# Performance work log

Measured on AMD Instinct MI355X. Metric: run time of the kernel, lower is better.

## Reference

```python
import jax, jax.numpy as jnp
import numpy as np

S, B, E, H, NQ, V, T = 128, 128, 64, 8, 8, 30000, 12
N_RAND_OPS = 30


def _build_random_layer(n_wires, n_ops=N_RAND_OPS, seed=1234):
    # Deterministic stand-in for tq.RandomLayer(n_ops=30): random fixed-angle
    # rotations and CNOTs over the wires.
    rng = np.random.RandomState(seed)
    ops = []
    for _ in range(n_ops):
        kind = rng.randint(4)
        if kind == 3 and n_wires >= 2:
            c = int(rng.randint(n_wires))
            t = int(rng.randint(n_wires - 1))
            if t >= c:
                t += 1
            ops.append(('cnot', c, t, 0.0))
        else:
            g = ('rx', 'ry', 'rz')[kind % 3]
            ops.append((g, int(rng.randint(n_wires)), -1, float(rng.uniform(0.0, 2 * np.pi))))
    return ops

_RAND_OPS = _build_random_layer(H)


def _apply_rot(state, kind, theta, w):
    # state: (N, 2, 2, ..., 2); wire w lives on axis w+1. theta: scalar or (N,).
    th = jnp.asarray(theta, jnp.float32)
    if th.ndim == 1:
        th = th.reshape((-1,) + (1,) * (state.ndim - 2))
    th = th / 2
    a0 = jnp.take(state, 0, axis=w + 1)
    a1 = jnp.take(state, 1, axis=w + 1)
    c, s = jnp.cos(th), jnp.sin(th)
    if kind == 'rx':
        n0, n1 = c * a0 - 1j * s * a1, -1j * s * a0 + c * a1
    elif kind == 'ry':
        n0, n1 = c * a0 - s * a1, s * a0 + c * a1
    else:  # rz
        p = jnp.exp(-1j * th)
        n0, n1 = p * a0, jnp.conj(p) * a1
    return jnp.stack([n0, n1], axis=w + 1)


def _apply_cnot(state, c, t):
    s0 = jnp.take(state, 0, axis=c + 1)
    s1 = jnp.take(state, 1, axis=c + 1)
    t_ax = t + 1 if t < c else t  # target axis after removing control axis
    s1 = jnp.flip(s1, axis=t_ax)
    return jnp.stack([s0, s1], axis=c + 1)


def _measure_z(state):
    probs = jnp.real(state * jnp.conj(state))
    n = state.ndim - 1
    zs = []
    for w in range(n):
        d = jnp.take(probs, 0, axis=w + 1) - jnp.take(probs, 1, axis=w + 1)
        zs.append(d.sum(axis=tuple(range(1, d.ndim))))
    return jnp.stack(zs, axis=1)  # (N, n_wires)


def setup_inputs() -> dict:
    key = jax.random.key(0)
    ks = jax.random.split(key, 10)
    fan_lin = E + H
    return {
        'emb': jax.random.normal(ks[0], (V, E), jnp.float32),
        'Win': jax.random.normal(ks[1], (4, NQ, fan_lin), jnp.float32) / np.sqrt(fan_lin),
        'b_in': jax.random.normal(ks[2], (4, NQ), jnp.float32) * 0.1,
        'phi': jax.random.uniform(ks[3], (4, NQ), jnp.float32, 0.0, 2 * np.pi),
        'Wout': jax.random.normal(ks[4], (4, H, NQ), jnp.float32) / np.sqrt(NQ),
        'b_out': jax.random.normal(ks[5], (4, H), jnp.float32) * 0.1,
        'phiq': jax.random.uniform(ks[6], (H,), jnp.float32, 0.0, 2 * np.pi),
        'Whead': jax.random.normal(ks[7], (T, H), jnp.float32) / np.sqrt(H),
        'b_head': jax.random.normal(ks[8], (T,), jnp.float32) * 0.1,
        'sentence': jax.random.randint(ks[9], (S, B), 0, V, jnp.int64),
    }


def reference(emb, Win, b_in, phi, Wout, b_out, phiq, Whead, b_head, sentence):
    embeds = emb[sentence]  # (S, B, E)
    bsz = sentence.shape[1]
    h0 = jnp.zeros((bsz, H), emb.dtype)
    c0 = jnp.zeros_like(h0)

    def step(carry, x):
        hx, cx = carry
        comb = jnp.concatenate([x, hx], axis=1)  # (B, E+H)
        # QGate closed form: RX(z_i) encode + trainable RX(phi_i) + CNOT chain
        # gives <Z_k> = prod_{j<=k} cos(z_j + phi_j).
        z = jnp.einsum('bf,gqf->bgq', comb, Win) + b_in + phi  # (B,4,NQ)
        q = jnp.cumprod(jnp.cos(z), axis=-1)
        pre = jnp.einsum('bgq,ghq->bgh', q, Wout) + b_out      # (B,4,H)
        f = jax.nn.sigmoid(pre[:, 0])
        i = jax.nn.sigmoid(pre[:, 1])
        g = jnp.tanh(pre[:, 2])
        o = jax.nn.sigmoid(pre[:, 3])
        cx = f * cx + i * g
        hx = o * jnp.tanh(cx)
        return (hx, cx), hx

    _, outs = jax.lax.scan(step, (h0, c0), embeds)  # (S, B, H)
    flat = outs.transpose(1, 0, 2).reshape(-1, H)   # (B*S, H) batch-major (as in source)

    # QFC head: statevector simulation over H wires
    n = H
    N = flat.shape[0]
    state = jnp.zeros((N, 2 ** n), jnp.complex64).at[:, 0].set(1.0)
    state = state.reshape((N,) + (2,) * n)
    for w in range(n):
        state = _apply_rot(state, 'ry', flat[:, w], w)
    for name, a, b, ang in _RAND_OPS:
        if name == 'cnot':
            state = _apply_cnot(state, a, b)
        else:
            state = _apply_rot(state, name, ang, a)
    for w in range(n):
        state = _apply_rot(state, 'rx', phiq[w], w)
    zexp = _measure_z(state)                        # (B*S, H)
    logits = zexp @ Whead.T + b_head
    # faithful to source: view batch-major flat tensor as (seq, batch, T)
    logits = logits.reshape(S, B, T)
    return jax.nn.log_softmax(logits, axis=2)
```

## Files before the change

kernel.cpp:

```cpp
#include <hip/hip_runtime.h>
#include <math.h>
#include <stdint.h>

#define S_    128
#define B_    128
#define E_    64
#define H_    8
#define T_    12
#define FAN_  72
#define NOPS_ 30
#define MAXG_ 30

constexpr double CT_PI = 3.14159265358979323846;

constexpr double ct_cos(double x) {
    double t = 1.0, s = 1.0, x2 = x * x;
    for (int k = 1; k <= 20; k++) { t *= -x2 / ((2.0*k - 1.0) * (2.0*k)); s += t; }
    return s;
}
constexpr double ct_sin(double x) {
    double t = x, s = x, x2 = x * x;
    for (int k = 1; k <= 20; k++) { t *= -x2 / ((2.0*k) * (2.0*k + 1.0)); s += t; }
    return s;
}

constexpr void ct_mmul(const double* A, const double* B, double* C) {
    for (int i = 0; i < 2; i++)
        for (int j = 0; j < 2; j++) {
            double rr = 0.0, ii = 0.0;
            for (int k = 0; k < 2; k++) {
                double ar = A[(i*2+k)*2], ai = A[(i*2+k)*2+1];
                double br = B[(k*2+j)*2], bi = B[(k*2+j)*2+1];
                rr += ar*br - ai*bi;
                ii += ar*bi + ai*br;
            }
            C[(i*2+j)*2] = rr; C[(i*2+j)*2+1] = ii;
        }
}

struct CTC {
    int n;
    int type[MAXG_];
    int w1[MAXG_];
    int w2[MAXG_];
    double U[MAXG_][8];
    double initM[8][8];
    double endM[8][8];
};

constexpr CTC build_ct() {
    uint32_t mt[624] = {};
    int idx = 624;
    {
        uint32_t s = 1234u;
        for (int i = 0; i < 624; i++) {
            mt[i] = s;
            s = 1812433253u * (s ^ (s >> 30)) + (uint32_t)i + 1u;
        }
    }
    auto nextf = [&]() -> uint32_t {
        if (idx >= 624) {
            for (int i = 0; i < 624; i++) {
                uint32_t y = (mt[i] & 0x80000000u) | (mt[(i+1)%624] & 0x7fffffffu);
                uint32_t v = mt[(i+397)%624] ^ (y >> 1);
                mt[i] = (y & 1u) ? (v ^ 0x9908b0dfu) : v;
            }
            idx = 0;
        }
        uint32_t y = mt[idx++];
        y ^= y >> 11;
        y ^= (y << 7)  & 0x9d2c5680u;
        y ^= (y << 15) & 0xefc60000u;
        y ^= y >> 18;
        return y;
    };
    auto randint = [&](uint32_t n) -> uint32_t {
        uint32_t rng = n - 1u, mask = rng;
        mask |= mask >> 1; mask |= mask >> 2; mask |= mask >> 4;
        mask |= mask >> 8; mask |= mask >> 16;
        uint32_t v = 0;
        do { v = nextf() & mask; } while (v > rng);
        return v;
    };
    auto uniform2pi = [&]() -> double {
        uint32_t a = nextf() >> 5;
        uint32_t b = nextf() >> 6;
        double d = ((double)a * 67108864.0 + (double)b) / 9007199254740992.0;
        return 2.0 * CT_PI * d;
    };

    int kindA[NOPS_] = {}, aA[NOPS_] = {}, bA[NOPS_] = {};
    double UA[NOPS_][8] = {};
    for (int i = 0; i < NOPS_; i++) {
        uint32_t kind = randint(4);
        if (kind == 3u) {
            int c = (int)randint(8);
            int t = (int)randint(7);
            if (t >= c) t += 1;
            kindA[i] = 1; aA[i] = c; bA[i] = t;
            UA[i][0] = 1.0; UA[i][6] = 1.0;
        } else {
            int g = (int)(kind % 3u);
            int w = (int)randint(8);
            double th = uniform2pi();
            double c = ct_cos(0.5 * th), s = ct_sin(0.5 * th);
            kindA[i] = 0; aA[i] = w; bA[i] = -1;
            if (g == 0)      { UA[i][0]=c;  UA[i][3]=-s; UA[i][5]=-s; UA[i][6]=c; }
            else if (g == 1) { UA[i][0]=c;  UA[i][2]=-s; UA[i][4]= s; UA[i][6]=c; }
            else             { UA[i][0]=c;  UA[i][1]=-s; UA[i][6]= c; UA[i][7]=s; }
        }
    }

    int ikind[MAXG_] = {}, ia[MAXG_] = {}, ib[MAXG_] = {};
    double iU[MAXG_][8] = {};
    int cnt = 0;
    double initM[8][8] = {}, endM[8][8] = {};
    for (int w = 0; w < 8; w++) { initM[w][0] = 1.0; initM[w][6] = 1.0;
                                  endM[w][0]  = 1.0; endM[w][6]  = 1.0; }

    for (int oi = 0; oi < NOPS_; oi++) {
        if (kindA[oi] == 0) {
            int w = aA[oi], k = cnt - 1;
            bool merged = false;
            while (k >= 0) {
                if (ikind[k] == 0) {
                    if (ia[k] == w) {
                        double tmp[8] = {};
                        ct_mmul(UA[oi], iU[k], tmp);
                        for (int j = 0; j < 8; j++) iU[k][j] = tmp[j];
                        merged = true; break;
                    }
                    k--;
                } else {
                    if (w == ia[k] || w == ib[k]) break;
                    k--;
                }
            }
            if (merged) continue;
            if (k < 0) {
                double tmp[8] = {};
                ct_mmul(UA[oi], initM[w], tmp);
                for (int j = 0; j < 8; j++) initM[w][j] = tmp[j];
                continue;
            }
            ikind[cnt] = 0; ia[cnt] = w; ib[cnt] = -1;
            for (int j = 0; j < 8; j++) iU[cnt][j] = UA[oi][j];
            cnt++;
        } else {
            int c = aA[oi], t2 = bA[oi], k = cnt - 1;
            bool cancelled = false;
            while (k >= 0) {
                if (ikind[k] == 0) {
                    int w = ia[k];
                    if (w == c || w == t2) break;
                    k--;
                } else {
                    int c2 = ia[k], tt = ib[k];
                    if (c2 == c && tt == t2) {
                        for (int m = k; m < cnt - 1; m++) {
                            ikind[m] = ikind[m+1]; ia[m] = ia[m+1]; ib[m] = ib[m+1];
                            for (int j = 0; j < 8; j++) iU[m][j] = iU[m+1][j];
                        }
                        cnt--; cancelled = true; break;
                    }
                    if (c2 != t2 && tt != c) k--;
                    else break;
                }
            }
            if (!cancelled) {
                ikind[cnt] = 1; ia[cnt] = c; ib[cnt] = t2;
                for (int j = 0; j < 8; j++) iU[cnt][j] = 0.0;
                iU[cnt][0] = 1.0; iU[cnt][6] = 1.0;
                cnt++;
            }
        }
    }
    bool blocked[8] = {};
    for (int k = cnt - 1; k >= 0; k--) {
        if (ikind[k] == 0) {
            int w = ia[k];
            if (!blocked[w]) {
                double tmp[8] = {};
                ct_mmul(endM[w], iU[k], tmp);
                for (int j = 0; j < 8; j++) endM[w][j] = tmp[j];
                for (int m = k; m < cnt - 1; m++) {
                    ikind[m] = ikind[m+1]; ia[m] = ia[m+1]; ib[m] = ib[m+1];
                    for (int j = 0; j < 8; j++) iU[m][j] = iU[m+1][j];
                }
                cnt--;
            }
        } else {
            blocked[ia[k]] = true; blocked[ib[k]] = true;
        }
    }

    CTC q = {};
    q.n = cnt;
    for (int i = 0; i < cnt; i++) {
        q.type[i] = ikind[i]; q.w1[i] = ia[i]; q.w2[i] = ib[i];
        for (int j = 0; j < 8; j++) q.U[i][j] = iU[i][j];
    }
    for (int w = 0; w < 8; w++)
        for (int j = 0; j < 8; j++) { q.initM[w][j] = initM[w][j]; q.endM[w][j] = endM[w][j]; }
    return q;
}

constexpr CTC CIRC = build_ct();

__device__ __forceinline__ float sigmoid_f(float x) { return 1.f / (1.f + __expf(-x)); }
__device__ __forceinline__ float tanh_f(float x) {
    float e = __expf(2.f * x);
    return 1.f - 2.f / (e + 1.f);
}

template<int CTRL>
__device__ __forceinline__ float dppf(float x) {
    union { float f; int i; } u, r;
    u.f = x;
    r.i = __builtin_amdgcn_update_dpp(0, u.i, CTRL, 0xF, 0xF, true);
    return r.f;
}

template<int M>
__device__ __forceinline__ float lane_xor(float x, int lane) {
    if constexpr (M == 1)  return dppf<0xB1>(x);
    else if constexpr (M == 2) return dppf<0x4E>(x);
    else if constexpr (M == 4) {
        float a = dppf<0x104>(x);
        float b = dppf<0x114>(x);
        return (lane & 4) ? b : a;
    }
    else if constexpr (M == 8) return dppf<0x128>(x);
    else return __shfl_xor(x, M, 64);
}

template<int W>
__device__ __forceinline__ float exch(float x, int lane) {
    if constexpr (W == 0) return __shfl_xor(x, 32, 64);
    else if constexpr (W == 1) return __shfl_xor(x, 16, 64);
    else if constexpr (W == 2) return lane_xor<8>(x, lane);
    else if constexpr (W == 3) return lane_xor<4>(x, lane);
    else if constexpr (W == 4) return lane_xor<2>(x, lane);
    else return lane_xor<1>(x, lane);
}

template<int W>
__device__ __forceinline__ int qbit_ct(int lane, int j) {
    if constexpr (W < 6) return (lane >> (5 - W)) & 1;
    else if constexpr (W == 6) return (j >> 1) & 1;
    else return j & 1;
}

__device__ __forceinline__ void pair_rt(float u0, float u1, float u2, float u3,
                                        float u4, float u5, float u6, float u7,
                                        float& a0r, float& a0i, float& a1r, float& a1i) {
    float n0r = u0*a0r - u1*a0i + u2*a1r - u3*a1i;
    float n0i = u0*a0i + u1*a0r + u2*a1i + u3*a1r;
    float n1r = u4*a0r - u5*a0i + u6*a1r - u7*a1i;
    float n1i = u4*a0i + u5*a0r + u6*a1i + u7*a1r;
    a0r = n0r; a0i = n0i; a1r = n1r; a1i = n1i;
}

template<int W>
__device__ __forceinline__ void gate_rt(float u0, float u1, float u2, float u3,
                                        float u4, float u5, float u6, float u7,
                                        int lane, float ar[4], float ai[4]) {
    if constexpr (W < 6) {
        const int b = (lane >> (5 - W)) & 1;
        const float dr  = b ? u6 : u0;
        const float di  = b ? u7 : u1;
        const float onr = b ? u4 : u2;
        const float oni = b ? u5 : u3;
        #pragma unroll
        for (int j = 0; j < 4; j++) {
            float br = exch<W>(ar[j], lane);
            float bi = exch<W>(ai[j], lane);
            float nr = dr * ar[j] - di * ai[j] + onr * br - oni * bi;
            float ni = dr * ai[j] + di * ar[j] + onr * bi + oni * br;
            ar[j] = nr; ai[j] = ni;
        }
    } else if constexpr (W == 6) {
        pair_rt(u0,u1,u2,u3,u4,u5,u6,u7, ar[0], ai[0], ar[2], ai[2]);
        pair_rt(u0,u1,u2,u3,u4,u5,u6,u7, ar[1], ai[1], ar[3], ai[3]);
    } else {
        pair_rt(u0,u1,u2,u3,u4,u5,u6,u7, ar[0], ai[0], ar[1], ai[1]);
        pair_rt(u0,u1,u2,u3,u4,u5,u6,u7, ar[2], ai[2], ar[3], ai[3]);
    }
}

template<int CW, int TW>
__device__ __forceinline__ void cnot_ct(int lane, float ar[4], float ai[4]) {
    if constexpr (TW < 6) {
        #pragma unroll
        for (int j = 0; j < 4; j++) {
            float br = exch<TW>(ar[j], lane);
            float bi = exch<TW>(ai[j], lane);
            int ctrl = qbit_ct<CW>(lane, j);
            ar[j] = ctrl ? br : ar[j];
            ai[j] = ctrl ? bi : ai[j];
        }
    } else if constexpr (TW == 6) {
        int cA = qbit_ct<CW>(lane, 0), cB = qbit_ct<CW>(lane, 1);
        float n0r = cA ? ar[2] : ar[0], n0i = cA ? ai[2] : ai[0];
        float n2r = cA ? ar[0] : ar[2], n2i = cA ? ai[0] : ai[2];
        float n1r = cB ? ar[3] : ar[1], n1i = cB ? ai[3] : ai[1];
        float n3r = cB ? ar[1] : ar[3], n3i = cB ? ai[1] : ai[3];
        ar[0]=n0r; ai[0]=n0i; ar[1]=n1r; ai[1]=n1i;
        ar[2]=n2r; ai[2]=n2i; ar[3]=n3r; ai[3]=n3i;
    } else {
        int cA = qbit_ct<CW>(lane, 0), cB = qbit_ct<CW>(lane, 2);
        float n0r = cA ? ar[1] : ar[0], n0i = cA ? ai[1] : ai[0];
        float n1r = cA ? ar[0] : ar[1], n1i = cA ? ai[0] : ai[1];
        float n2r = cB ? ar[3] : ar[2], n2i = cB ? ai[3] : ai[2];
        float n3r = cB ? ar[2] : ar[3], n3i = cB ? ai[2] : ai[3];
        ar[0]=n0r; ai[0]=n0i; ar[1]=n1r; ai[1]=n1i;
        ar[2]=n2r; ai[2]=n2i; ar[3]=n3r; ai[3]=n3i;
    }
}

template<int I>
__device__ __forceinline__ void gate_op(int lane, float ar[4], float ai[4]) {
    constexpr int w = CIRC.w1[I];
    constexpr float u0 = (float)CIRC.U[I][0], u1 = (float)CIRC.U[I][1];
    constexpr float u2 = (float)CIRC.U[I][2], u3 = (float)CIRC.U[I][3];
    constexpr float u4 = (float)CIRC.U[I][4], u5 = (float)CIRC.U[I][5];
    constexpr float u6 = (float)CIRC.U[I][6], u7 = (float)CIRC.U[I][7];
    gate_rt<w>(u0,u1,u2,u3,u4,u5,u6,u7, lane, ar, ai);
}

template<int I>
__device__ __forceinline__ void run_ops(int lane, float ar[4], float ai[4]) {
    if constexpr (I < CIRC.n) {
        if constexpr (CIRC.type[I] == 0) gate_op<I>(lane, ar, ai);
        else cnot_ct<CIRC.w1[I], CIRC.w2[I]>(lane, ar, ai);
        run_ops<I + 1>(lane, ar, ai);
    }
}

struct V2 { float r0, i0, r1, i1; };
template<int W>
__device__ __forceinline__ V2 init_wire(float th) {
    constexpr float m0 = (float)CIRC.initM[W][0], m1 = (float)CIRC.initM[W][1];
    constexpr float m2 = (float)CIRC.initM[W][2], m3 = (float)CIRC.initM[W][3];
    constexpr float m4 = (float)CIRC.initM[W][4], m5 = (float)CIRC.initM[W][5];
    constexpr float m6 = (float)CIRC.initM[W][6], m7 = (float)CIRC.initM[W][7];
    float c = __cosf(th), s = __sinf(th);
    V2 v;
    v.r0 = m0*c + m2*s; v.i0 = m1*c + m3*s;
    v.r1 = m4*c + m6*s; v.i1 = m5*c + m7*s;
    return v;
}

template<int W>
__device__ __forceinline__ void final_wire(float c, float s, int lane,
                                           float ar[4], float ai[4]) {
    constexpr float E0 = (float)CIRC.endM[W][0], E1 = (float)CIRC.endM[W][1];
    constexpr float E2 = (float)CIRC.endM[W][2], E3 = (float)CIRC.endM[W][3];
    constexpr float E4 = (float)CIRC.endM[W][4], E5 = (float)CIRC.endM[W][5];
    constexpr float E6 = (float)CIRC.endM[W][6], E7 = (float)CIRC.endM[W][7];
    float F0 =  c*E0 + s*E5;
    float F1 =  c*E1 - s*E4;
    float F2 =  c*E2 + s*E7;
    float F3 =  c*E3 - s*E6;
    float F4 =  s*E1 + c*E4;
    float F5 = -s*E0 + c*E5;
    float F6 =  s*E3 + c*E6;
    float F7 = -s*E2 + c*E7;
    gate_rt<W>(F0,F1,F2,F3,F4,F5,F6,F7, lane, ar, ai);
}

__device__ __forceinline__ void bcast8(float v, int lane, float h[8]) {
    float p  = lane_xor<1>(v, lane);
    float a0 = (lane & 1) ? p : v;
    float a1 = (lane & 1) ? v : p;
    float q0 = lane_xor<2>(a0, lane);
    float q1 = lane_xor<2>(a1, lane);
    float b0 = (lane & 2) ? q0 : a0;
    float b1 = (lane & 2) ? q1 : a1;
    float b2 = (lane & 2) ? a0 : q0;
    float b3 = (lane & 2) ? a1 : q1;
    float r0 = lane_xor<4>(b0, lane);
    float r1 = lane_xor<4>(b1, lane);
    float r2 = lane_xor<4>(b2, lane);
    float r3 = lane_xor<4>(b3, lane);
    h[0] = (lane & 4) ? r0 : b0;  h[1] = (lane & 4) ? r1 : b1;
    h[2] = (lane & 4) ? r2 : b2;  h[3] = (lane & 4) ? r3 : b3;
    h[4] = (lane & 4) ? b0 : r0;  h[5] = (lane & 4) ? b1 : r1;
    h[6] = (lane & 4) ? b2 : r2;  h[7] = (lane & 4) ? b3 : r3;
}

__global__ __launch_bounds__(1024) void k_fused(
    const float* __restrict__ emb,
    const int* __restrict__ sentence,
    const float* __restrict__ Win,
    const float* __restrict__ b_in,
    const float* __restrict__ phi,
    const float* __restrict__ Wout,
    const float* __restrict__ b_out,
    const float* __restrict__ phiq,
    const float* __restrict__ Whead,
    const float* __restrict__ b_head,
    float* __restrict__ out)
{
    __shared__ float zxs[S_][32];
    __shared__ float sang[S_][8];

    const int t     = threadIdx.x;
    const int wave  = t >> 6;
    const int lane  = t & 63;
    const int half  = lane >> 5;
    const int l     = lane & 31;
    const int b     = blockIdx.x >> 1;
    const int half3 = blockIdx.x & 1;

    {
        const float4* w4 = (const float4*)(Win + l * FAN_);
        const float cb = b_in[l] + phi[l];

        const float4* e4_0;
        const float4* e4_1;
        const float4* e4_2;
        const float4* e4_3;
        {
            const int s0 = wave * 8 + 0 + half;
            const int s1 = wave * 8 + 2 + half;
            const int s2 = wave * 8 + 4 + half;
            const int s3 = wave * 8 + 6 + half;
            e4_0 = (const float4*)(emb + sentence[s0 * B_ + b] * E_);
            e4_1 = (const float4*)(emb + sentence[s1 * B_ + b] * E_);
            e4_2 = (const float4*)(emb + sentence[s2 * B_ + b] * E_);
            e4_3 = (const float4*)(emb + sentence[s3 * B_ + b] * E_);
        }
        float a0 = cb, a1 = cb, a2 = cb, a3 = cb;
        #pragma unroll
        for (int f = 0; f < 16; f++) {
            float4 wv = w4[f];
            float4 x0 = e4_0[f];
            float4 x1 = e4_1[f];
            float4 x2 = e4_2[f];
            float4 x3 = e4_3[f];
            a0 = fmaf(x0.x, wv.x, a0); a0 = fmaf(x0.y, wv.y, a0);
            a0 = fmaf(x0.z, wv.z, a0); a0 = fmaf(x0.w, wv.w, a0);
            a1 = fmaf(x1.x, wv.x, a1); a1 = fmaf(x1.y, wv.y, a1);
            a1 = fmaf(x1.z, wv.z, a1); a1 = fmaf(x1.w, wv.w, a1);
            a2 = fmaf(x2.x, wv.x, a2); a2 = fmaf(x2.y, wv.y, a2);
            a2 = fmaf(x2.z, wv.z, a2); a2 = fmaf(x2.w, wv.w, a2);
            a3 = fmaf(x3.x, wv.x, a3); a3 = fmaf(x3.y, wv.y, a3);
            a3 = fmaf(x3.z, wv.z, a3); a3 = fmaf(x3.w, wv.w, a3);
        }
        zxs[wave * 8 + 0 + half][l] = a0;
        zxs[wave * 8 + 2 + half][l] = a1;
        zxs[wave * 8 + 4 + half][l] = a2;
        zxs[wave * 8 + 6 + half][l] = a3;
    }
    __syncthreads();

    if (t < 32) {
        const int g = t >> 3;
        const int h = t & 7;
        const int q = t & 7;
        float wh[8], wo[8];
        #pragma unroll
        for (int k = 0; k < 8; k++) wh[k] = Win[t * FAN_ + 64 + k];
        #pragma unroll
        for (int k = 0; k < 8; k++) wo[k] = Wout[(g * 8 + h) * 8 + k];
        const float bo = b_out[g * 8 + h];

        float hxv[8];
        #pragma unroll
        for (int k = 0; k < 8; k++) hxv[k] = 0.f;
        float cx = 0.f;

        for (int s = 0; s < S_; s++) {
            float z = zxs[s][t];
            #pragma unroll
            for (int k = 0; k < 8; k++) z = fmaf(wh[k], hxv[k], z);

            float qc = __cosf(z);
            float u1 = dppf<0x111>(qc); qc = (q >= 1) ? qc * u1 : qc;
            float u2 = dppf<0x112>(qc); qc = (q >= 2) ? qc * u2 : qc;
            float u4 = dppf<0x114>(qc); qc = (q >= 4) ? qc * u4 : qc;

            float qch[8];
            bcast8(qc, t, qch);
            float pre = bo;
            #pragma unroll
            for (int qq = 0; qq < 8; qq++) pre = fmaf(wo[qq], qch[qq], pre);

            float e1 = lane_xor<8>(pre, t);
            float e2 = __shfl_xor(pre, 16, 64);
            float e3 = __shfl_xor(e1, 16, 64);
            float p0 = (g==0)?pre:(g==1)?e1:(g==2)?e2:e3;
            float p1 = (g==1)?pre:(g==0)?e1:(g==3)?e2:e3;
            float p2 = (g==2)?pre:(g==3)?e1:(g==0)?e2:e3;
            float p3 = (g==3)?pre:(g==2)?e1:(g==1)?e2:e3;

            float f_ = sigmoid_f(p0);
            float i_ = sigmoid_f(p1);
            float g_ = tanh_f(p2);
            float o_ = sigmoid_f(p3);
            cx = f_ * cx + i_ * g_;
            float hnew = o_ * tanh_f(cx);

            if (t < 8) sang[s][t] = hnew;
            bcast8(hnew, t, hxv);
        }
    }
    __syncthreads();

    float cq0 = __cosf(phiq[0]*0.5f), sq0 = __sinf(phiq[0]*0.5f);
    float cq1 = __cosf(phiq[1]*0.5f), sq1 = __sinf(phiq[1]*0.5f);
    float cq2 = __cosf(phiq[2]*0.5f), sq2 = __sinf(phiq[2]*0.5f);
    float cq3 = __cosf(phiq[3]*0.5f), sq3 = __sinf(phiq[3]*0.5f);
    float cq4 = __cosf(phiq[4]*0.5f), sq4 = __sinf(phiq[4]*0.5f);
    float cq5 = __cosf(phiq[5]*0.5f), sq5 = __sinf(phiq[5]*0.5f);
    float cq6 = __cosf(phiq[6]*0.5f), sq6 = __sinf(phiq[6]*0.5f);
    float cq7 = __cosf(phiq[7]*0.5f), sq7 = __sinf(phiq[7]*0.5f);

    for (int r = 0; r < 4; r++) {
        const int s = half3 * 64 + wave * 4 + r;

        float ar[4], ai[4];
        {
            V2 v0 = init_wire<0>(sang[s][0] * 0.5f);
            V2 v1 = init_wire<1>(sang[s][1] * 0.5f);
            V2 v2 = init_wire<2>(sang[s][2] * 0.5f);
            V2 v3 = init_wire<3>(sang[s][3] * 0.5f);
            V2 v4 = init_wire<4>(sang[s][4] * 0.5f);
            V2 v5 = init_wire<5>(sang[s][5] * 0.5f);
            V2 v6 = init_wire<6>(sang[s][6] * 0.5f);
            V2 v7 = init_wire<7>(sang[s][7] * 0.5f);
            float Pr = 1.f, Pi = 0.f;
            {
                int bit = (lane >> 5) & 1;
                float er = bit ? v0.r1 : v0.r0, ei = bit ? v0.i1 : v0.i0;
                float nr = Pr*er - Pi*ei, ni = Pr*ei + Pi*er; Pr = nr; Pi = ni;
            }
            {
                int bit = (lane >> 4) & 1;
                float er = bit ? v1.r1 : v1.r0, ei = bit ? v1.i1 : v1.i0;
                float nr = Pr*er - Pi*ei, ni = Pr*ei + Pi*er; Pr = nr; Pi = ni;
            }
            {
                int bit = (lane >> 3) & 1;
                float er = bit ? v2.r1 : v2.r0, ei = bit ? v2.i1 : v2.i0;
                float nr = Pr*er - Pi*ei, ni = Pr*ei + Pi*er; Pr = nr; Pi = ni;
            }
            {
                int bit = (lane >> 2) & 1;
                float er = bit ? v3.r1 : v3.r0, ei = bit ? v3.i1 : v3.i0;
                float nr = Pr*er - Pi*ei, ni = Pr*ei + Pi*er; Pr = nr; Pi = ni;
            }
            {
                int bit = (lane >> 1) & 1;
                float er = bit ? v4.r1 : v4.r0, ei = bit ? v4.i1 : v4.i0;
                float nr = Pr*er - Pi*ei, ni = Pr*ei + Pi*er; Pr = nr; Pi = ni;
            }
            {
                int bit = lane & 1;
                float er = bit ? v5.r1 : v5.r0, ei = bit ? v5.i1 : v5.i0;
                float nr = Pr*er - Pi*ei, ni = Pr*ei + Pi*er; Pr = nr; Pi = ni;
            }
            float t0r = Pr*v6.r0 - Pi*v6.i0, t0i = Pr*v6.i0 + Pi*v6.r0;
            float t1r = Pr*v6.r1 - Pi*v6.i1, t1i = Pr*v6.i1 + Pi*v6.r1;
            ar[0] = t0r*v7.r0 - t0i*v7.i0;  ai[0] = t0r*v7.i0 + t0i*v7.r0;
            ar[1] = t0r*v7.r1 - t0i*v7.i1;  ai[1] = t0r*v7.i1 + t0i*v7.r1;
            ar[2] = t1r*v7.r0 - t1i*v7.i0;  ai[2] = t1r*v7.i0 + t1i*v7.r0;
            ar[3] = t1r*v7.r1 - t1i*v7.i1;  ai[3] = t1r*v7.i1 + t1i*v7.r1;
        }

        run_ops<0>(lane, ar, ai);

        final_wire<0>(cq0, sq0, lane, ar, ai);
        final_wire<1>(cq1, sq1, lane, ar, ai);
        final_wire<2>(cq2, sq2, lane, ar, ai);
        final_wire<3>(cq3, sq3, lane, ar, ai);
        final_wire<4>(cq4, sq4, lane, ar, ai);
        final_wire<5>(cq5, sq5, lane, ar, ai);
        final_wire<6>(cq6, sq6, lane, ar, ai);
        final_wire<7>(cq7, sq7, lane, ar, ai);

        float p0 = ar[0]*ar[0] + ai[0]*ai[0];
        float p1 = ar[1]*ar[1] + ai[1]*ai[1];
        float p2 = ar[2]*ar[2] + ai[2]*ai[2];
        float p3 = ar[3]*ar[3] + ai[3]*ai[3];
        float pt = p0 + p1 + p2 + p3;
        float a6 = p0 + p1 - p2 - p3;
        float a7 = p0 - p1 + p2 - p3;
        {
            float tv;
            tv = lane_xor<1>(pt, lane);  pt = (lane & 1)  ? (tv - pt) : (tv + pt);
            tv = lane_xor<2>(pt, lane);  pt = (lane & 2)  ? (tv - pt) : (tv + pt);
            tv = lane_xor<4>(pt, lane);  pt = (lane & 4)  ? (tv - pt) : (tv + pt);
            tv = lane_xor<8>(pt, lane);  pt = (lane & 8)  ? (tv - pt) : (tv + pt);
            tv = lane_xor<16>(pt, lane); pt = (lane & 16) ? (tv - pt) : (tv + pt);
            tv = lane_xor<32>(pt, lane); pt = (lane & 32) ? (tv - pt) : (tv + pt);
            a6 += lane_xor<1>(a6, lane);  a6 += lane_xor<2>(a6, lane);
            a6 += lane_xor<4>(a6, lane);  a6 += lane_xor<8>(a6, lane);
            a6 += lane_xor<16>(a6, lane); a6 += lane_xor<32>(a6, lane);
            a7 += lane_xor<1>(a7, lane);  a7 += lane_xor<2>(a7, lane);
            a7 += lane_xor<4>(a7, lane);  a7 += lane_xor<8>(a7, lane);
            a7 += lane_xor<16>(a7, lane); a7 += lane_xor<32>(a7, lane);
        }
        float zl[8];
        zl[0] = __shfl(pt, 32, 64);
        zl[1] = __shfl(pt, 16, 64);
        zl[2] = __shfl(pt, 8, 64);
        zl[3] = __shfl(pt, 4, 64);
        zl[4] = __shfl(pt, 2, 64);
        zl[5] = __shfl(pt, 1, 64);
        zl[6] = a6;
        zl[7] = a7;

        float logit = -1e30f;
        if (lane < T_) {
            logit = b_head[lane];
            #pragma unroll
            for (int w = 0; w < 8; w++)
                logit = fmaf(zl[w], Whead[lane * 8 + w], logit);
        }
        float mx = logit;
        mx = fmaxf(mx, lane_xor<1>(mx, lane));
        mx = fmaxf(mx, lane_xor<2>(mx, lane));
        mx = fmaxf(mx, lane_xor<4>(mx, lane));
        mx = fmaxf(mx, lane_xor<8>(mx, lane));
        float e = (lane < T_) ? __expf(logit - mx) : 0.f;
        float se = e;
        se += lane_xor<1>(se, lane);
        se += lane_xor<2>(se, lane);
        se += lane_xor<4>(se, lane);
        se += lane_xor<8>(se, lane);
        if (lane < T_)
            out[(b * S_ + s) * T_ + lane] = logit - mx - __logf(se);
    }
}

extern "C" void kernel_launch(void* const* d_in, const int* in_sizes, int n_in,
                              void* d_out, int out_size, void* d_ws, size_t ws_size,
                              hipStream_t stream)
{
    (void)in_sizes; (void)n_in; (void)out_size; (void)d_ws; (void)ws_size;
    const float* emb    = (const float*)d_in[0];
    const float* Win    = (const float*)d_in[1];
    const float* b_in   = (const float*)d_in[2];
    const float* phi    = (const float*)d_in[3];
    const float* Wout   = (const float*)d_in[4];
    const float* b_out  = (const float*)d_in[5];
    const float* phiq   = (const float*)d_in[6];
    const float* Whead  = (const float*)d_in[7];
    const float* b_head = (const float*)d_in[8];
    const int* sentence = (const int*)d_in[9];
    float* out          = (float*)d_out;

    hipLaunchKernelGGL(k_fused, dim3(2 * B_), dim3(1024), 0, stream,
                       emb, sentence, Win, b_in, phi, Wout, b_out,
                       phiq, Whead, b_head, out);
}
```

Baseline: 172.2 us.

## Split fused LSTM+QFC kernel into separate recurrence and quantum-head kernels via workspace

When enough workspace is available, the single fused kernel is replaced by two launches. The first runs the serial LSTM recurrence once per batch element in a 256-thread block and writes the angles to global memory. The second is a wide kernel with 4 waves per block and 2 rows per wave that simulates the QFC statevector for all rows. This stops the 2x-redundant recurrence and the mostly idle 1024-thread blocks from sitting behind the serial part, and spreads the QFC work across the whole GPU, at the cost of a global round trip and an extra launch.

Measured after the change: 191.2 us. 11.0% more time.

```diff
diff --git a/kernel.cpp b/kernel.cpp
--- a/kernel.cpp
+++ b/kernel.cpp
@@ -10,6 +10,7 @@
 #define FAN_  72
 #define NOPS_ 30
 #define MAXG_ 30
+#define NROWS_ (S_ * B_)
 
 constexpr double CT_PI = 3.14159265358979323846;
 
@@ -389,6 +390,259 @@
     h[6] = (lane & 4) ? b2 : r2;  h[7] = (lane & 4) ? b3 : r3;
 }
 
+__device__ __forceinline__ void qfc_row(const float th[8],
+    float cq[8], float sq[8], int lane,
+    const float* __restrict__ Whead, const float* __restrict__ b_head,
+    float* __restrict__ outrow)
+{
+    float ar[4], ai[4];
+    {
+        V2 v0 = init_wire<0>(th[0]);
+        V2 v1 = init_wire<1>(th[1]);
+        V2 v2 = init_wire<2>(th[2]);
+        V2 v3 = init_wire<3>(th[3]);
+        V2 v4 = init_wire<4>(th[4]);
+        V2 v5 = init_wire<5>(th[5]);
+        V2 v6 = init_wire<6>(th[6]);
+        V2 v7 = init_wire<7>(th[7]);
+        float Pr = 1.f, Pi = 0.f;
+        {
+            int bit = (lane >> 5) & 1;
+            float er = bit ? v0.r1 : v0.r0, ei = bit ? v0.i1 : v0.i0;
+            float nr = Pr*er - Pi*ei, ni = Pr*ei + Pi*er; Pr = nr; Pi = ni;
+        }
+        {
+            int bit = (lane >> 4) & 1;
+            float er = bit ? v1.r1 : v1.r0, ei = bit ? v1.i1 : v1.i0;
+            float nr = Pr*er - Pi*ei, ni = Pr*ei + Pi*er; Pr = nr; Pi = ni;
+        }
+        {
+            int bit = (lane >> 3) & 1;
+            float er = bit ? v2.r1 : v2.r0, ei = bit ? v2.i1 : v2.i0;
+            float nr = Pr*er - Pi*ei, ni = Pr*ei + Pi*er; Pr = nr; Pi = ni;
+        }
+        {
+            int bit = (lane >> 2) & 1;
+            float er = bit ? v3.r1 : v3.r0, ei = bit ? v3.i1 : v3.i0;
+            float nr = Pr*er - Pi*ei, ni = Pr*ei + Pi*er; Pr = nr; Pi = ni;
+        }
+        {
+            int bit = (lane >> 1) & 1;
+            float er = bit ? v4.r1 : v4.r0, ei = bit ? v4.i1 : v4.i0;
+            float nr = Pr*er - Pi*ei, ni = Pr*ei + Pi*er; Pr = nr; Pi = ni;
+        }
+        {
+            int bit = lane & 1;
+            float er = bit ? v5.r1 : v5.r0, ei = bit ? v5.i1 : v5.i0;
+            float nr = Pr*er - Pi*ei, ni = Pr*ei + Pi*er; Pr = nr; Pi = ni;
+        }
+        float t0r = Pr*v6.r0 - Pi*v6.i0, t0i = Pr*v6.i0 + Pi*v6.r0;
+        float t1r = Pr*v6.r1 - Pi*v6.i1, t1i = Pr*v6.i1 + Pi*v6.r1;
+        ar[0] = t0r*v7.r0 - t0i*v7.i0;  ai[0] = t0r*v7.i0 + t0i*v7.r0;
+        ar[1] = t0r*v7.r1 - t0i*v7.i1;  ai[1] = t0r*v7.i1 + t0i*v7.r1;
+        ar[2] = t1r*v7.r0 - t1i*v7.i0;  ai[2] = t1r*v7.i0 + t1i*v7.r0;
+        ar[3] = t1r*v7.r1 - t1i*v7.i1;  ai[3] = t1r*v7.i1 + t1i*v7.r1;
+    }
+
+    run_ops<0>(lane, ar, ai);
+
+    final_wire<0>(cq[0], sq[0], lane, ar, ai);
+    final_wire<1>(cq[1], sq[1], lane, ar, ai);
+    final_wire<2>(cq[2], sq[2], lane, ar, ai);
+    final_wire<3>(cq[3], sq[3], lane, ar, ai);
+    final_wire<4>(cq[4], sq[4], lane, ar, ai);
+    final_wire<5>(cq[5], sq[5], lane, ar, ai);
+    final_wire<6>(cq[6], sq[6], lane, ar, ai);
+    final_wire<7>(cq[7], sq[7], lane, ar, ai);
+
+    float p0 = ar[0]*ar[0] + ai[0]*ai[0];
+    float p1 = ar[1]*ar[1] + ai[1]*ai[1];
+    float p2 = ar[2]*ar[2] + ai[2]*ai[2];
+    float p3 = ar[3]*ar[3] + ai[3]*ai[3];
+    float pt = p0 + p1 + p2 + p3;
+    float a6 = p0 + p1 - p2 - p3;
+    float a7 = p0 - p1 + p2 - p3;
+    {
+        float tv;
+        tv = lane_xor<1>(pt, lane);  pt = (lane & 1)  ? (tv - pt) : (tv + pt);
+        tv = lane_xor<2>(pt, lane);  pt = (lane & 2)  ? (tv - pt) : (tv + pt);
+        tv = lane_xor<4>(pt, lane);  pt = (lane & 4)  ? (tv - pt) : (tv + pt);
+        tv = lane_xor<8>(pt, lane);  pt = (lane & 8)  ? (tv - pt) : (tv + pt);
+        tv = lane_xor<16>(pt, lane); pt = (lane & 16) ? (tv - pt) : (tv + pt);
+        tv = lane_xor<32>(pt, lane); pt = (lane & 32) ? (tv - pt) : (tv + pt);
+        a6 += lane_xor<1>(a6, lane);  a6 += lane_xor<2>(a6, lane);
+        a6 += lane_xor<4>(a6, lane);  a6 += lane_xor<8>(a6, lane);
+        a6 += lane_xor<16>(a6, lane); a6 += lane_xor<32>(a6, lane);
+        a7 += lane_xor<1>(a7, lane);  a7 += lane_xor<2>(a7, lane);
+        a7 += lane_xor<4>(a7, lane);  a7 += lane_xor<8>(a7, lane);
+        a7 += lane_xor<16>(a7, lane); a7 += lane_xor<32>(a7, lane);
+    }
+    float zl[8];
+    zl[0] = __shfl(pt, 32, 64);
+    zl[1] = __shfl(pt, 16, 64);
+    zl[2] = __shfl(pt, 8, 64);
+    zl[3] = __shfl(pt, 4, 64);
+    zl[4] = __shfl(pt, 2, 64);
+    zl[5] = __shfl(pt, 1, 64);
+    zl[6] = a6;
+    zl[7] = a7;
+
+    float logit = -1e30f;
+    if (lane < T_) {
+        logit = b_head[lane];
+        #pragma unroll
+        for (int w = 0; w < 8; w++)
+            logit = fmaf(zl[w], Whead[lane * 8 + w], logit);
+    }
+    float mx = logit;
+    mx = fmaxf(mx, lane_xor<1>(mx, lane));
+    mx = fmaxf(mx, lane_xor<2>(mx, lane));
+    mx = fmaxf(mx, lane_xor<4>(mx, lane));
+    mx = fmaxf(mx, lane_xor<8>(mx, lane));
+    float e = (lane < T_) ? __expf(logit - mx) : 0.f;
+    float se = e;
+    se += lane_xor<1>(se, lane);
+    se += lane_xor<2>(se, lane);
+    se += lane_xor<4>(se, lane);
+    se += lane_xor<8>(se, lane);
+    if (lane < T_)
+        outrow[lane] = logit - mx - __logf(se);
+}
+
+__global__ __launch_bounds__(256) void k_lstm(
+    const float* __restrict__ emb,
+    const int* __restrict__ sentence,
+    const float* __restrict__ Win,
+    const float* __restrict__ b_in,
+    const float* __restrict__ phi,
+    const float* __restrict__ Wout,
+    const float* __restrict__ b_out,
+    float* __restrict__ angles)
+{
+    __shared__ float zxs[S_][32];
+
+    const int t  = threadIdx.x;
+    const int hw = t >> 5;
+    const int l  = t & 31;
+    const int b  = blockIdx.x;
+
+    {
+        const float4* w4 = (const float4*)(Win + l * FAN_);
+        const float cb = b_in[l] + phi[l];
+
+        #pragma unroll
+        for (int kk = 0; kk < 4; kk++) {
+            const int sb = hw * 16 + kk * 4;
+            const float4* e4_0 = (const float4*)(emb + sentence[(sb + 0) * B_ + b] * E_);
+            const float4* e4_1 = (const float4*)(emb + sentence[(sb + 1) * B_ + b] * E_);
+            const float4* e4_2 = (const float4*)(emb + sentence[(sb + 2) * B_ + b] * E_);
+            const float4* e4_3 = (const float4*)(emb + sentence[(sb + 3) * B_ + b] * E_);
+            float a0 = cb, a1 = cb, a2 = cb, a3 = cb;
+            #pragma unroll
+            for (int f = 0; f < 16; f++) {
+                float4 wv = w4[f];
+                float4 x0 = e4_0[f];
+                float4 x1 = e4_1[f];
+                float4 x2 = e4_2[f];
+                float4 x3 = e4_3[f];
+                a0 = fmaf(x0.x, wv.x, a0); a0 = fmaf(x0.y, wv.y, a0);
+                a0 = fmaf(x0.z, wv.z, a0); a0 = fmaf(x0.w, wv.w, a0);
+                a1 = fmaf(x1.x, wv.x, a1); a1 = fmaf(x1.y, wv.y, a1);
+                a1 = fmaf(x1.z, wv.z, a1); a1 = fmaf(x1.w, wv.w, a1);
+                a2 = fmaf(x2.x, wv.x, a2); a2 = fmaf(x2.y, wv.y, a2);
+                a2 = fmaf(x2.z, wv.z, a2); a2 = fmaf(x2.w, wv.w, a2);
+                a3 = fmaf(x3.x, wv.x, a3); a3 = fmaf(x3.y, wv.y, a3);
+                a3 = fmaf(x3.z, wv.z, a3); a3 = fmaf(x3.w, wv.w, a3);
+            }
+            zxs[sb + 0][l] = a0;
+            zxs[sb + 1][l] = a1;
+            zxs[sb + 2][l] = a2;
+            zxs[sb + 3][l] = a3;
+        }
+    }
+    __syncthreads();
+
+    if (t < 32) {
+        const int g = t >> 3;
+        const int h = t & 7;
+        const int q = t & 7;
+        float wh[8], wo[8];
+        #pragma unroll
+        for (int k = 0; k < 8; k++) wh[k] = Win[t * FAN_ + 64 + k];
+        #pragma unroll
+        for (int k = 0; k < 8; k++) wo[k] = Wout[(g * 8 + h) * 8 + k];
+        const float bo = b_out[g * 8 + h];
+
+        float hxv[8];
+        #pragma unroll
+        for (int k = 0; k < 8; k++) hxv[k] = 0.f;
+        float cx = 0.f;
+
+        for (int s = 0; s < S_; s++) {
+            float z = zxs[s][t];
+            #pragma unroll
+            for (int k = 0; k < 8; k++) z = fmaf(wh[k], hxv[k], z);
+
+            float qc = __cosf(z);
+            float u1 = dppf<0x111>(qc); qc = (q >= 1) ? qc * u1 : qc;
+            float u2 = dppf<0x112>(qc); qc = (q >= 2) ? qc * u2 : qc;
+            float u4 = dppf<0x114>(qc); qc = (q >= 4) ? qc * u4 : qc;
+
+            float qch[8];
+            bcast8(qc, t, qch);
+            float pre = bo;
+            #pragma unroll
+            for (int qq = 0; qq < 8; qq++) pre = fmaf(wo[qq], qch[qq], pre);
+
+            float e1 = lane_xor<8>(pre, t);
+            float e2 = __shfl_xor(pre, 16, 64);
+            float e3 = __shfl_xor(e1, 16, 64);
+            float p0 = (g==0)?pre:(g==1)?e1:(g==2)?e2:e3;
+            float p1 = (g==1)?pre:(g==0)?e1:(g==3)?e2:e3;
+            float p2 = (g==2)?pre:(g==3)?e1:(g==0)?e2:e3;
+            float p3 = (g==3)?pre:(g==2)?e1:(g==1)?e2:e3;
+
+            float f_ = sigmoid_f(p0);
+            float i_ = sigmoid_f(p1);
+            float g_ = tanh_f(p2);
+            float o_ = sigmoid_f(p3);
+            cx = f_ * cx + i_ * g_;
+            float hnew = o_ * tanh_f(cx);
+
+            if (t < 8) angles[(b * S_ + s) * 8 + t] = hnew;
+            bcast8(hnew, t, hxv);
+        }
+    }
+}
+
+__global__ __launch_bounds__(256) void k_qfc(
+    const float* __restrict__ angles,
+    const float* __restrict__ phiq,
+    const float* __restrict__ Whead,
+    const float* __restrict__ b_head,
+    float* __restrict__ out)
+{
+    const int t      = threadIdx.x;
+    const int lane   = t & 63;
+    const int waveId = blockIdx.x * 4 + (t >> 6);
+
+    float cq[8], sq[8];
+    #pragma unroll
+    for (int w = 0; w < 8; w++) {
+        float ph = phiq[w] * 0.5f;
+        cq[w] = __cosf(ph); sq[w] = __sinf(ph);
+    }
+
+    #pragma unroll
+    for (int rr = 0; rr < 2; rr++) {
+        const int row = waveId * 2 + rr;
+        float th[8];
+        #pragma unroll
+        for (int w = 0; w < 8; w++) th[w] = angles[row * 8 + w] * 0.5f;
+        qfc_row(th, cq, sq, lane, Whead, b_head, out + row * T_);
+    }
+}
+
 __global__ __launch_bounds__(1024) void k_fused(
     const float* __restrict__ emb,
     const int* __restrict__ sentence,
@@ -416,21 +670,14 @@
     {
         const float4* w4 = (const float4*)(Win + l * FAN_);
         const float cb = b_in[l] + phi[l];
-
-        const float4* e4_0;
-        const float4* e4_1;
-        const float4* e4_2;
-        const float4* e4_3;
-        {
-            const int s0 = wave * 8 + 0 + half;
-            const int s1 = wave * 8 + 2 + half;
-            const int s2 = wave * 8 + 4 + half;
-            const int s3 = wave * 8 + 6 + half;
-            e4_0 = (const float4*)(emb + sentence[s0 * B_ + b] * E_);
-            e4_1 = (const float4*)(emb + sentence[s1 * B_ + b] * E_);
-            e4_2 = (const float4*)(emb + sentence[s2 * B_ + b] * E_);
-            e4_3 = (const float4*)(emb + sentence[s3 * B_ + b] * E_);
-        }
+        const int s0 = wave * 8 + 0 + half;
+        const int s1 = wave * 8 + 2 + half;
+        const int s2 = wave * 8 + 4 + half;
+        const int s3 = wave * 8 + 6 + half;
+        const float4* e4_0 = (const float4*)(emb + sentence[s0 * B_ + b] * E_);
+        const float4* e4_1 = (const float4*)(emb + sentence[s1 * B_ + b] * E_);
+        const float4* e4_2 = (const float4*)(emb + sentence[s2 * B_ + b] * E_);
+        const float4* e4_3 = (const float4*)(emb + sentence[s3 * B_ + b] * E_);
         float a0 = cb, a1 = cb, a2 = cb, a3 = cb;
         #pragma unroll
         for (int f = 0; f < 16; f++) {
@@ -448,10 +695,10 @@
             a3 = fmaf(x3.x, wv.x, a3); a3 = fmaf(x3.y, wv.y, a3);
             a3 = fmaf(x3.z, wv.z, a3); a3 = fmaf(x3.w, wv.w, a3);
         }
-        zxs[wave * 8 + 0 + half][l] = a0;
-        zxs[wave * 8 + 2 + half][l] = a1;
-        zxs[wave * 8 + 4 + half][l] = a2;
-        zxs[wave * 8 + 6 + half][l] = a3;
+        zxs[s0][l] = a0;
+        zxs[s1][l] = a1;
+        zxs[s2][l] = a2;
+        zxs[s3][l] = a3;
     }
     __syncthreads();
 
@@ -508,130 +755,19 @@
     }
     __syncthreads();
 
-    float cq0 = __cosf(phiq[0]*0.5f), sq0 = __sinf(phiq[0]*0.5f);
-    float cq1 = __cosf(phiq[1]*0.5f), sq1 = __sinf(phiq[1]*0.5f);
-    float cq2 = __cosf(phiq[2]*0.5f), sq2 = __sinf(phiq[2]*0.5f);
-    float cq3 = __cosf(phiq[3]*0.5f), sq3 = __sinf(phiq[3]*0.5f);
-    float cq4 = __cosf(phiq[4]*0.5f), sq4 = __sinf(phiq[4]*0.5f);
-    float cq5 = __cosf(phiq[5]*0.5f), sq5 = __sinf(phiq[5]*0.5f);
-    float cq6 = __cosf(phiq[6]*0.5f), sq6 = __sinf(phiq[6]*0.5f);
-    float cq7 = __cosf(phiq[7]*0.5f), sq7 = __sinf(phiq[7]*0.5f);
+    float cq[8], sq[8];
+    #pragma unroll
+    for (int w = 0; w < 8; w++) {
+        float ph = phiq[w] * 0.5f;
+        cq[w] = __cosf(ph); sq[w] = __sinf(ph);
+    }
 
     for (int r = 0; r < 4; r++) {
         const int s = half3 * 64 + wave * 4 + r;
-
-        float ar[4], ai[4];
-        {
-            V2 v0 = init_wire<0>(sang[s][0] * 0.5f);
-            V2 v1 = init_wire<1>(sang[s][1] * 0.5f);
-            V2 v2 = init_wire<2>(sang[s][2] * 0.5f);
-            V2 v3 = init_wire<3>(sang[s][3] * 0.5f);
-            V2 v4 = init_wire<4>(sang[s][4] * 0.5f);
-            V2 v5 = init_wire<5>(sang[s][5] * 0.5f);
-            V2 v6 = init_wire<6>(sang[s][6] * 0.5f);
-            V2 v7 = init_wire<7>(sang[s][7] * 0.5f);
-            float Pr = 1.f, Pi = 0.f;
-            {
-                int bit = (lane >> 5) & 1;
-                float er = bit ? v0.r1 : v0.r0, ei = bit ? v0.i1 : v0.i0;
-                float nr = Pr*er - Pi*ei, ni = Pr*ei + Pi*er; Pr = nr; Pi = ni;
-            }
-            {
-                int bit = (lane >> 4) & 1;
-                float er = bit ? v1.r1 : v1.r0, ei = bit ? v1.i1 : v1.i0;
-                float nr = Pr*er - Pi*ei, ni = Pr*ei + Pi*er; Pr = nr; Pi = ni;
-            }
-            {
-                int bit = (lane >> 3) & 1;
-                float er = bit ? v2.r1 : v2.r0, ei = bit ? v2.i1 : v2.i0;
-                float nr = Pr*er - Pi*ei, ni = Pr*ei + Pi*er; Pr = nr; Pi = ni;
-            }
-            {
-                int bit = (lane >> 2) & 1;
-                float er = bit ? v3.r1 : v3.r0, ei = bit ? v3.i1 : v3.i0;
-                float nr = Pr*er - Pi*ei, ni = Pr*ei + Pi*er; Pr = nr; Pi = ni;
-            }
-            {
-                int bit = (lane >> 1) & 1;
-                float er = bit ? v4.r1 : v4.r0, ei = bit ? v4.i1 : v4.i0;
-                float nr = Pr*er - Pi*ei, ni = Pr*ei + Pi*er; Pr = nr; Pi = ni;
-            }
-            {
-                int bit = lane & 1;
-                float er = bit ? v5.r1 : v5.r0, ei = bit ? v5.i1 : v5.i0;
-                float nr = Pr*er - Pi*ei, ni = Pr*ei + Pi*er; Pr = nr; Pi = ni;
-            }
-            float t0r = Pr*v6.r0 - Pi*v6.i0, t0i = Pr*v6.i0 + Pi*v6.r0;
-            float t1r = Pr*v6.r1 - Pi*v6.i1, t1i = Pr*v6.i1 + Pi*v6.r1;
-            ar[0] = t0r*v7.r0 - t0i*v7.i0;  ai[0] = t0r*v7.i0 + t0i*v7.r0;
-            ar[1] = t0r*v7.r1 - t0i*v7.i1;  ai[1] = t0r*v7.i1 + t0i*v7.r1;
-            ar[2] = t1r*v7.r0 - t1i*v7.i0;  ai[2] = t1r*v7.i0 + t1i*v7.r0;
-            ar[3] = t1r*v7.r1 - t1i*v7.i1;  ai[3] = t1r*v7.i1 + t1i*v7.r1;
-        }
-
-        run_ops<0>(lane, ar, ai);
-
-        final_wire<0>(cq0, sq0, lane, ar, ai);
-        final_wire<1>(cq1, sq1, lane, ar, ai);
-        final_wire<2>(cq2, sq2, lane, ar, ai);
-        final_wire<3>(cq3, sq3, lane, ar, ai);
-        final_wire<4>(cq4, sq4, lane, ar, ai);
-        final_wire<5>(cq5, sq5, lane, ar, ai);
-        final_wire<6>(cq6, sq6, lane, ar, ai);
-        final_wire<7>(cq7, sq7, lane, ar, ai);
-
-        float p0 = ar[0]*ar[0] + ai[0]*ai[0];
-        float p1 = ar[1]*ar[1] + ai[1]*ai[1];
-        float p2 = ar[2]*ar[2] + ai[2]*ai[2];
-        float p3 = ar[3]*ar[3] + ai[3]*ai[3];
-        float pt = p0 + p1 + p2 + p3;
-        float a6 = p0 + p1 - p2 - p3;
-        float a7 = p0 - p1 + p2 - p3;
-        {
-            float tv;
-            tv = lane_xor<1>(pt, lane);  pt = (lane & 1)  ? (tv - pt) : (tv + pt);
-            tv = lane_xor<2>(pt, lane);  pt = (lane & 2)  ? (tv - pt) : (tv + pt);
-            tv = lane_xor<4>(pt, lane);  pt = (lane & 4)  ? (tv - pt) : (tv + pt);
-            tv = lane_xor<8>(pt, lane);  pt = (lane & 8)  ? (tv - pt) : (tv + pt);
-            tv = lane_xor<16>(pt, lane); pt = (lane & 16) ? (tv - pt) : (tv + pt);
-            tv = lane_xor<32>(pt, lane); pt = (lane & 32) ? (tv - pt) : (tv + pt);
-            a6 += lane_xor<1>(a6, lane);  a6 += lane_xor<2>(a6, lane);
-            a6 += lane_xor<4>(a6, lane);  a6 += lane_xor<8>(a6, lane);
-            a6 += lane_xor<16>(a6, lane); a6 += lane_xor<32>(a6, lane);
-            a7 += lane_xor<1>(a7, lane);  a7 += lane_xor<2>(a7, lane);
-            a7 += lane_xor<4>(a7, lane);  a7 += lane_xor<8>(a7, lane);
-            a7 += lane_xor<16>(a7, lane); a7 += lane_xor<32>(a7, lane);
-        }
-        float zl[8];
-        zl[0] = __shfl(pt, 32, 64);
-        zl[1] = __shfl(pt, 16, 64);
-        zl[2] = __shfl(pt, 8, 64);
-        zl[3] = __shfl(pt, 4, 64);
-        zl[4] = __shfl(pt, 2, 64);
-        zl[5] = __shfl(pt, 1, 64);
-        zl[6] = a6;
-        zl[7] = a7;
-
-        float logit = -1e30f;
-        if (lane < T_) {
-            logit = b_head[lane];
-            #pragma unroll
-            for (int w = 0; w < 8; w++)
-                logit = fmaf(zl[w], Whead[lane * 8 + w], logit);
-        }
-        float mx = logit;
-        mx = fmaxf(mx, lane_xor<1>(mx, lane));
-        mx = fmaxf(mx, lane_xor<2>(mx, lane));
-        mx = fmaxf(mx, lane_xor<4>(mx, lane));
-        mx = fmaxf(mx, lane_xor<8>(mx, lane));
-        float e = (lane < T_) ? __expf(logit - mx) : 0.f;
-        float se = e;
-        se += lane_xor<1>(se, lane);
-        se += lane_xor<2>(se, lane);
-        se += lane_xor<4>(se, lane);
-        se += lane_xor<8>(se, lane);
-        if (lane < T_)
-            out[(b * S_ + s) * T_ + lane] = logit - mx - __logf(se);
+        float th[8];
+        #pragma unroll
+        for (int w = 0; w < 8; w++) th[w] = sang[s][w] * 0.5f;
+        qfc_row(th, cq, sq, lane, Whead, b_head, out + (b * S_ + s) * T_);
     }
 }
 
@@ -639,7 +775,7 @@
                               void* d_out, int out_size, void* d_ws, size_t ws_size,
                               hipStream_t stream)
 {
-    (void)in_sizes; (void)n_in; (void)out_size; (void)d_ws; (void)ws_size;
+    (void)in_sizes; (void)n_in; (void)out_size;
     const float* emb    = (const float*)d_in[0];
     const float* Win    = (const float*)d_in[1];
     const float* b_in   = (const float*)d_in[2];
@@ -652,7 +788,16 @@
     const int* sentence = (const int*)d_in[9];
     float* out          = (float*)d_out;
 
-    hipLaunchKernelGGL(k_fused, dim3(2 * B_), dim3(1024), 0, stream,
-                       emb, sentence, Win, b_in, phi, Wout, b_out,
-                       phiq, Whead, b_head, out);
-}
+    const size_t need = (size_t)NROWS_ * 8 * sizeof(float);
+    if (ws_size >= need) {
+        float* angles = (float*)d_ws;
+        hipLaunchKernelGGL(k_lstm, dim3(B_), dim3(256), 0, stream,
+                           emb, sentence, Win, b_in, phi, Wout, b_out, angles);
+        hipLaunchKernelGGL(k_qfc, dim3(NROWS_ / 8), dim3(256), 0, stream,
+                           angles, phiq, Whead, b_head, out);
+    } else {
+        hipLaunchKernelGGL(k_fused, dim3(2 * B_), dim3(1024), 0, stream,
+                           emb, sentence, Win, b_in, phi, Wout, b_out,
+                           phiq, Whead, b_head, out);
+    }
+}
```
